# Optimization experiments

Hardware: AMD Instinct MI355X
Metric: run time of the kernel (lower is better)

The kernel has to match this reference:

```python
import jax, jax.numpy as jnp
import numpy as np

# --- static configuration (mirrors init_kwargs) ---
L = 16        # latent_size
HL = 512      # hypernet_layer_size
D = 64        # decoder_layer_size
NDEC = 2      # decoder_n_layers
B, G = 128, 100  # batch, grid (pressure levels)
LOGP_MEAN, LOGP_STD = 0.0, 3.0
T_MEAN, T_STD = 1500.0, 500.0

# decoder layer structure generated by the hypernet
WEIGHT_SIZES = [(1, D)] + [(D, D)] * NDEC + [(D, 1)]
BIAS_SIZES = [1] + [D] * NDEC + [1]
OUT_SIZE = sum(a * b for a, b in WEIGHT_SIZES) + sum(BIAS_SIZES)  # 8450


def setup_inputs() -> dict:
    key = jax.random.key(0)
    ks = jax.random.split(key, 8)
    def init(k, shape, fan_in):
        return (jax.random.normal(k, shape, jnp.float32) / np.float32(np.sqrt(fan_in)))
    return {
        "z": jax.random.normal(ks[0], (B, L), jnp.float32),
        "log_P": jax.random.normal(ks[1], (B, G), jnp.float32) * 2.0,
        # hypernet MLP params: L -> HL -> HL -> HL -> OUT_SIZE
        "hW0": init(ks[2], (L, HL), L), "hb0": jnp.zeros((HL,), jnp.float32),
        "hW1": init(ks[3], (HL, HL), HL), "hb1": jnp.zeros((HL,), jnp.float32),
        "hW2": init(ks[4], (HL, HL), HL), "hb2": jnp.zeros((HL,), jnp.float32),
        "hWo": init(ks[5], (HL, OUT_SIZE), HL), "hbo": jnp.zeros((OUT_SIZE,), jnp.float32),
    }


def reference(z, log_P, hW0, hb0, hW1, hb1, hW2, hb2, hWo, hbo):
    Bsz, Gsz = log_P.shape
    R = Bsz * Gsz  # flattened rows
    # broadcast latent over the pressure grid: (B, L) -> (R, L)
    z_flat = jnp.broadcast_to(z[:, None, :], (Bsz, Gsz, z.shape[-1])).reshape(R, -1)
    # normalize pressure -> decoder input, shape (R, 1)
    x = (log_P.reshape(R, 1) - LOGP_MEAN) / LOGP_STD
    # hypernet MLP (leaky_relu, slope 0.01 like torch default)
    h = jax.nn.leaky_relu(z_flat @ hW0 + hb0)
    h = jax.nn.leaky_relu(h @ hW1 + hb1)
    h = jax.nn.leaky_relu(h @ hW2 + hb2)
    wab = h @ hWo + hbo  # (R, OUT_SIZE): per-row decoder weights+biases
    # per-row decoder: chain of batched GEMVs with siren activation
    off = 0
    n_layers = len(WEIGHT_SIZES)
    for i, ((di, do), bs) in enumerate(zip(WEIGHT_SIZES, BIAS_SIZES)):
        n = di * do
        w = wab[:, off:off + n].reshape(R, di, do)
        b = wab[:, off + n:off + n + bs]  # broadcasts against (R, do)
        off += n + bs
        x = jnp.einsum('bi,bij->bj', x, w) + b
        if i == 0:
            x = x * 30.0  # siren first-layer omega_0
        if i < n_layers - 1:
            x = jnp.sin(x)  # siren activation; last layer is Identity
    T_pred = x.reshape(Bsz, Gsz)
    # undo temperature normalization
    return T_pred * T_STD + T_MEAN
```

## Files before the change

kernel.cpp:

```cpp
#include <hip/hip_runtime.h>

#define WSTRIDE 8704
#define GSTR 65

__device__ __forceinline__ float lrelu(float x) { return x > 0.0f ? x : 0.01f * x; }

__global__ __launch_bounds__(128) void h0T_kernel(const float* __restrict__ z,
                                                  const float* __restrict__ W,
                                                  const float* __restrict__ bias,
                                                  float* __restrict__ h0T) {
    int j = blockIdx.x;
    int b = threadIdx.x;
    float zr[16];
    *(float4*)&zr[0]  = *(const float4*)&z[b * 16 + 0];
    *(float4*)&zr[4]  = *(const float4*)&z[b * 16 + 4];
    *(float4*)&zr[8]  = *(const float4*)&z[b * 16 + 8];
    *(float4*)&zr[12] = *(const float4*)&z[b * 16 + 12];
    float acc = bias[j];
#pragma unroll
    for (int l = 0; l < 16; ++l) acc = fmaf(zr[l], W[l * 512 + j], acc);
    h0T[j * 128 + b] = lrelu(acc);
}

__global__ __launch_bounds__(256) void gemmT_kernel(const float* __restrict__ At,
                                                    const float* __restrict__ W,
                                                    const float* __restrict__ bias,
                                                    float* __restrict__ OT) {
    __shared__ __align__(16) float As[512][4];
    __shared__ float red[4][64][5];
    int jt = blockIdx.x & 7;
    int bt = blockIdx.x >> 3;
    int tid = threadIdx.x;
    int lane = tid & 63;
    int wid  = __builtin_amdgcn_readfirstlane(tid >> 6);
    int b0 = bt * 4;
#pragma unroll
    for (int r = 0; r < 4; ++r) {
        int p = r * 256 + tid;
        int k = p >> 1, q = p & 1;
        *(float2*)&As[k][q * 2] = *(const float2*)&At[k * 128 + b0 + q * 2];
    }
    __syncthreads();
    int j = jt * 64 + lane;
    float acc[4] = {};
    int k0 = wid * 128;
#pragma unroll 8
    for (int kk = 0; kk < 128; ++kk) {
        int k = k0 + kk;
        float4 a = *(const float4*)&As[k][0];
        float w = W[k * 512 + j];
        acc[0] = fmaf(a.x, w, acc[0]);
        acc[1] = fmaf(a.y, w, acc[1]);
        acc[2] = fmaf(a.z, w, acc[2]);
        acc[3] = fmaf(a.w, w, acc[3]);
    }
#pragma unroll
    for (int i = 0; i < 4; ++i) red[wid][lane][i] = acc[i];
    __syncthreads();
    int jj = tid >> 2;
    int bb = tid & 3;
    float s = red[0][jj][bb] + red[1][jj][bb] + red[2][jj][bb] + red[3][jj][bb];
    int jg = jt * 64 + jj;
    OT[jg * 128 + b0 + bb] = lrelu(s + bias[jg]);
}

__global__ __launch_bounds__(256) void wabT_kernel(const float* __restrict__ At,
                                                   const float* __restrict__ W,
                                                   const float* __restrict__ bias,
                                                   float* __restrict__ wab) {
    __shared__ __align__(16) float As[512][16];
    __shared__ float red[4][64][33];
    int tid = threadIdx.x;
    if (blockIdx.x == 528) {
        int b = tid & 127;
        int jc = 8448 + (tid >> 7);
        float a0 = 0.f, a1 = 0.f, a2 = 0.f, a3 = 0.f;
#pragma unroll 4
        for (int k4 = 0; k4 < 128; ++k4) {
            a0 = fmaf(At[(k4*4+0) * 128 + b], W[(k4*4+0) * 8450 + jc], a0);
            a1 = fmaf(At[(k4*4+1) * 128 + b], W[(k4*4+1) * 8450 + jc], a1);
            a2 = fmaf(At[(k4*4+2) * 128 + b], W[(k4*4+2) * 8450 + jc], a2);
            a3 = fmaf(At[(k4*4+3) * 128 + b], W[(k4*4+3) * 8450 + jc], a3);
        }
        wab[b * WSTRIDE + jc] = a0 + a1 + a2 + a3 + bias[jc];
        return;
    }
    int v = (blockIdx.x & 7) * 66 + (blockIdx.x >> 3);
    int jt = v >> 3;
    int bt = v & 7;
    int lane = tid & 63;
    int wid  = __builtin_amdgcn_readfirstlane(tid >> 6);
    int b0 = bt * 16;
#pragma unroll
    for (int r = 0; r < 16; ++r) {
        int p = r * 256 + tid;
        int k = p >> 3, q = p & 7;
        *(float2*)&As[k][q * 2] = *(const float2*)&At[k * 128 + b0 + q * 2];
    }
    __syncthreads();
    int j0 = jt * 128 + lane * 2;
    float acc[16][2] = {};
    int k0 = wid * 128;
#pragma unroll 4
    for (int kk = 0; kk < 128; ++kk) {
        int k = k0 + kk;
        float4 a0 = *(const float4*)&As[k][0];
        float4 a1 = *(const float4*)&As[k][4];
        float4 a2 = *(const float4*)&As[k][8];
        float4 a3 = *(const float4*)&As[k][12];
        float2 w = *(const float2*)&W[k * 8450 + j0];
        float av[16] = {a0.x,a0.y,a0.z,a0.w, a1.x,a1.y,a1.z,a1.w,
                        a2.x,a2.y,a2.z,a2.w, a3.x,a3.y,a3.z,a3.w};
#pragma unroll
        for (int bb = 0; bb < 16; ++bb) {
            acc[bb][0] = fmaf(av[bb], w.x, acc[bb][0]);
            acc[bb][1] = fmaf(av[bb], w.y, acc[bb][1]);
        }
    }
#pragma unroll
    for (int bb = 0; bb < 16; ++bb) {
        red[wid][lane][bb * 2 + 0] = acc[bb][0];
        red[wid][lane][bb * 2 + 1] = acc[bb][1];
    }
    __syncthreads();
    int jj = tid >> 1;
    int bh = tid & 1;
    int lane_r = jj >> 1;
    int jl = jj & 1;
    int jg = jt * 128 + jj;
    float bj = bias[jg];
#pragma unroll
    for (int bq = 0; bq < 8; ++bq) {
        int bb = bh * 8 + bq;
        int idx = bb * 2 + jl;
        float s = red[0][lane_r][idx] + red[1][lane_r][idx]
                + red[2][lane_r][idx] + red[3][lane_r][idx];
        wab[(b0 + bb) * WSTRIDE + jg] = s + bj;
    }
}

__global__ __launch_bounds__(256) void decoder_kernel(const float* __restrict__ wab,
                                                      const float* __restrict__ logP,
                                                      float* __restrict__ out) {
    __shared__ __align__(16) float Wl[64 * 64];
    __shared__ float hX[64 * GSTR];
    __shared__ float hY[64 * GSTR];
    __shared__ float red[4][68];
    int b   = blockIdx.x >> 1;
    int gbl = blockIdx.x & 1;
    int tid = threadIdx.x;
    int lane = tid & 63;
    int wid  = __builtin_amdgcn_readfirstlane(tid >> 6);
    int jq = wid * 16;
    int g = gbl * 64 + lane;
    bool act = g < 100;
    const float* __restrict__ row = wab + b * WSTRIDE;
    float x0 = act ? logP[b * 100 + g] * (1.0f / 3.0f) : 0.0f;

    float c0 = row[64];
#pragma unroll
    for (int t = 0; t < 16; ++t)
        hX[(jq + t) * GSTR + lane] = __sinf(30.0f * fmaf(x0, row[jq + t], c0));
#pragma unroll
    for (int r = 0; r < 16; ++r) {
        int idx = r * 256 + tid;
        Wl[idx] = row[65 + idx];
    }
    __syncthreads();

    {
        float a[16];
#pragma unroll
        for (int t = 0; t < 16; ++t) a[t] = row[4161 + jq + t];
#pragma unroll 4
        for (int i = 0; i < 64; ++i) {
            float hi = hX[i * GSTR + lane];
            const float* wr = &Wl[i * 64 + jq];
            float4 w0 = *(const float4*)&wr[0];
            float4 w1 = *(const float4*)&wr[4];
            float4 w2 = *(const float4*)&wr[8];
            float4 w3 = *(const float4*)&wr[12];
            a[0]  = fmaf(hi, w0.x, a[0]);  a[1]  = fmaf(hi, w0.y, a[1]);
            a[2]  = fmaf(hi, w0.z, a[2]);  a[3]  = fmaf(hi, w0.w, a[3]);
            a[4]  = fmaf(hi, w1.x, a[4]);  a[5]  = fmaf(hi, w1.y, a[5]);
            a[6]  = fmaf(hi, w1.z, a[6]);  a[7]  = fmaf(hi, w1.w, a[7]);
            a[8]  = fmaf(hi, w2.x, a[8]);  a[9]  = fmaf(hi, w2.y, a[9]);
            a[10] = fmaf(hi, w2.z, a[10]); a[11] = fmaf(hi, w2.w, a[11]);
            a[12] = fmaf(hi, w3.x, a[12]); a[13] = fmaf(hi, w3.y, a[13]);
            a[14] = fmaf(hi, w3.z, a[14]); a[15] = fmaf(hi, w3.w, a[15]);
        }
#pragma unroll
        for (int t = 0; t < 16; ++t) hY[(jq + t) * GSTR + lane] = __sinf(a[t]);
    }
    __syncthreads();
#pragma unroll
    for (int r = 0; r < 16; ++r) {
        int idx = r * 256 + tid;
        Wl[idx] = row[4225 + idx];
    }
    __syncthreads();

    {
        float a[16];
#pragma unroll
        for (int t = 0; t < 16; ++t) a[t] = row[8321 + jq + t];
#pragma unroll 4
        for (int i = 0; i < 64; ++i) {
            float hi = hY[i * GSTR + lane];
            const float* wr = &Wl[i * 64 + jq];
            float4 w0 = *(const float4*)&wr[0];
            float4 w1 = *(const float4*)&wr[4];
            float4 w2 = *(const float4*)&wr[8];
            float4 w3 = *(const float4*)&wr[12];
            a[0]  = fmaf(hi, w0.x, a[0]);  a[1]  = fmaf(hi, w0.y, a[1]);
            a[2]  = fmaf(hi, w0.z, a[2]);  a[3]  = fmaf(hi, w0.w, a[3]);
            a[4]  = fmaf(hi, w1.x, a[4]);  a[5]  = fmaf(hi, w1.y, a[5]);
            a[6]  = fmaf(hi, w1.z, a[6]);  a[7]  = fmaf(hi, w1.w, a[7]);
            a[8]  = fmaf(hi, w2.x, a[8]);  a[9]  = fmaf(hi, w2.y, a[9]);
            a[10] = fmaf(hi, w2.z, a[10]); a[11] = fmaf(hi, w2.w, a[11]);
            a[12] = fmaf(hi, w3.x, a[12]); a[13] = fmaf(hi, w3.y, a[13]);
            a[14] = fmaf(hi, w3.z, a[14]); a[15] = fmaf(hi, w3.w, a[15]);
        }
#pragma unroll
        for (int t = 0; t < 16; ++t) hX[(jq + t) * GSTR + lane] = __sinf(a[t]);
    }
    __syncthreads();

    float p = 0.f;
#pragma unroll
    for (int t = 0; t < 16; ++t)
        p = fmaf(hX[(jq + t) * GSTR + lane], row[8385 + jq + t], p);
    red[wid][lane] = p;
    __syncthreads();
    if (wid == 0 && act) {
        float s = red[0][lane] + red[1][lane] + red[2][lane] + red[3][lane] + row[8449];
        out[b * 100 + g] = fmaf(s, 500.0f, 1500.0f);
    }
}

extern "C" void kernel_launch(void* const* d_in, const int* in_sizes, int n_in,
                              void* d_out, int out_size, void* d_ws, size_t ws_size,
                              hipStream_t stream) {
    const float* z    = (const float*)d_in[0];
    const float* logP = (const float*)d_in[1];
    const float* hW0  = (const float*)d_in[2];
    const float* hb0  = (const float*)d_in[3];
    const float* hW1  = (const float*)d_in[4];
    const float* hb1  = (const float*)d_in[5];
    const float* hW2  = (const float*)d_in[6];
    const float* hb2  = (const float*)d_in[7];
    const float* hWo  = (const float*)d_in[8];
    const float* hbo  = (const float*)d_in[9];
    float* out = (float*)d_out;

    float* wab = (float*)d_ws;
    float* h0T = wab + 128 * WSTRIDE;
    float* h1T = h0T + 512 * 128;
    float* h2T = h1T + 512 * 128;

    h0T_kernel<<<512, 128, 0, stream>>>(z, hW0, hb0, h0T);
    gemmT_kernel<<<256, 256, 0, stream>>>(h0T, hW1, hb1, h1T);
    gemmT_kernel<<<256, 256, 0, stream>>>(h1T, hW2, hb2, h2T);
    wabT_kernel<<<529, 256, 0, stream>>>(h2T, hWo, hbo, wab);
    decoder_kernel<<<256, 256, 0, stream>>>(wab, logP, out);
}
```

Baseline: 72.71 us.

## Double threads in gemm/decoder, software-pipeline wab GEMM, fold tail columns into tiles

The hidden-layer GEMMs and the decoder now use 512-thread blocks, so each wave handles half the K range or half the output columns, with a wider final reduction. The wab GEMM inner loop is restructured into a double-buffered register pipeline that prefetches the next 4-k group of shared-memory A values and global W values while computing the current one. It also gets a 2-blocks-per-SIMD launch bound. The special block for the two leftover columns is replaced by an extra tile-column with clamped loads and guarded stores. Together these aim to raise parallelism and hide load latency, at the cost of more registers in the wab kernel and more reduction work.

New measurement: 61.08 us. 16.0% less time.

```diff
diff --git a/kernel.cpp b/kernel.cpp
--- a/kernel.cpp
+++ b/kernel.cpp
@@ -22,12 +22,12 @@
     h0T[j * 128 + b] = lrelu(acc);
 }
 
-__global__ __launch_bounds__(256) void gemmT_kernel(const float* __restrict__ At,
+__global__ __launch_bounds__(512) void gemmT_kernel(const float* __restrict__ At,
                                                     const float* __restrict__ W,
                                                     const float* __restrict__ bias,
                                                     float* __restrict__ OT) {
     __shared__ __align__(16) float As[512][4];
-    __shared__ float red[4][64][5];
+    __shared__ float red[8][64][5];
     int jt = blockIdx.x & 7;
     int bt = blockIdx.x >> 3;
     int tid = threadIdx.x;
@@ -35,17 +35,17 @@
     int wid  = __builtin_amdgcn_readfirstlane(tid >> 6);
     int b0 = bt * 4;
 #pragma unroll
-    for (int r = 0; r < 4; ++r) {
-        int p = r * 256 + tid;
+    for (int r = 0; r < 2; ++r) {
+        int p = r * 512 + tid;
         int k = p >> 1, q = p & 1;
         *(float2*)&As[k][q * 2] = *(const float2*)&At[k * 128 + b0 + q * 2];
     }
     __syncthreads();
     int j = jt * 64 + lane;
     float acc[4] = {};
-    int k0 = wid * 128;
+    int k0 = wid * 64;
 #pragma unroll 8
-    for (int kk = 0; kk < 128; ++kk) {
+    for (int kk = 0; kk < 64; ++kk) {
         int k = k0 + kk;
         float4 a = *(const float4*)&As[k][0];
         float w = W[k * 512 + j];
@@ -57,35 +57,57 @@
 #pragma unroll
     for (int i = 0; i < 4; ++i) red[wid][lane][i] = acc[i];
     __syncthreads();
-    int jj = tid >> 2;
-    int bb = tid & 3;
-    float s = red[0][jj][bb] + red[1][jj][bb] + red[2][jj][bb] + red[3][jj][bb];
-    int jg = jt * 64 + jj;
-    OT[jg * 128 + b0 + bb] = lrelu(s + bias[jg]);
-}
-
-__global__ __launch_bounds__(256) void wabT_kernel(const float* __restrict__ At,
-                                                   const float* __restrict__ W,
-                                                   const float* __restrict__ bias,
-                                                   float* __restrict__ wab) {
+    if (tid < 256) {
+        int jj = tid >> 2;
+        int bb = tid & 3;
+        float s = 0.f;
+#pragma unroll
+        for (int w = 0; w < 8; ++w) s += red[w][jj][bb];
+        int jg = jt * 64 + jj;
+        OT[jg * 128 + b0 + bb] = lrelu(s + bias[jg]);
+    }
+}
+
+__device__ __forceinline__ void loadg(const float As[][16], const float* __restrict__ W,
+                                      int k0, int g, int j0,
+                                      float4 (&aa)[4][4], float2 (&ww)[4]) {
+    int kb = k0 + g * 4;
+#pragma unroll
+    for (int kk = 0; kk < 4; ++kk) {
+        const float* asr = As[kb + kk];
+        aa[kk][0] = *(const float4*)&asr[0];
+        aa[kk][1] = *(const float4*)&asr[4];
+        aa[kk][2] = *(const float4*)&asr[8];
+        aa[kk][3] = *(const float4*)&asr[12];
+        ww[kk] = *(const float2*)&W[(kb + kk) * 8450 + j0];
+    }
+}
+
+__device__ __forceinline__ void compg(const float4 (&aa)[4][4], const float2 (&ww)[4],
+                                      float (&acc)[16][2]) {
+#pragma unroll
+    for (int kk = 0; kk < 4; ++kk) {
+#pragma unroll
+        for (int q = 0; q < 4; ++q) {
+            const float4 a = aa[kk][q];
+            const float av[4] = {a.x, a.y, a.z, a.w};
+#pragma unroll
+            for (int e = 0; e < 4; ++e) {
+                acc[q * 4 + e][0] = fmaf(av[e], ww[kk].x, acc[q * 4 + e][0]);
+                acc[q * 4 + e][1] = fmaf(av[e], ww[kk].y, acc[q * 4 + e][1]);
+            }
+        }
+    }
+}
+
+__global__ __launch_bounds__(256, 2) void wabT_kernel(const float* __restrict__ At,
+                                                      const float* __restrict__ W,
+                                                      const float* __restrict__ bias,
+                                                      float* __restrict__ wab) {
     __shared__ __align__(16) float As[512][16];
     __shared__ float red[4][64][33];
     int tid = threadIdx.x;
-    if (blockIdx.x == 528) {
-        int b = tid & 127;
-        int jc = 8448 + (tid >> 7);
-        float a0 = 0.f, a1 = 0.f, a2 = 0.f, a3 = 0.f;
-#pragma unroll 4
-        for (int k4 = 0; k4 < 128; ++k4) {
-            a0 = fmaf(At[(k4*4+0) * 128 + b], W[(k4*4+0) * 8450 + jc], a0);
-            a1 = fmaf(At[(k4*4+1) * 128 + b], W[(k4*4+1) * 8450 + jc], a1);
-            a2 = fmaf(At[(k4*4+2) * 128 + b], W[(k4*4+2) * 8450 + jc], a2);
-            a3 = fmaf(At[(k4*4+3) * 128 + b], W[(k4*4+3) * 8450 + jc], a3);
-        }
-        wab[b * WSTRIDE + jc] = a0 + a1 + a2 + a3 + bias[jc];
-        return;
-    }
-    int v = (blockIdx.x & 7) * 66 + (blockIdx.x >> 3);
+    int v = (blockIdx.x & 7) * 67 + (blockIdx.x >> 3);
     int jt = v >> 3;
     int bt = v & 7;
     int lane = tid & 63;
@@ -98,25 +120,22 @@
         *(float2*)&As[k][q * 2] = *(const float2*)&At[k * 128 + b0 + q * 2];
     }
     __syncthreads();
-    int j0 = jt * 128 + lane * 2;
+    int j0r = jt * 128 + lane * 2;
+    int j0 = j0r < 8448 ? j0r : 8448;
     float acc[16][2] = {};
     int k0 = wid * 128;
-#pragma unroll 4
-    for (int kk = 0; kk < 128; ++kk) {
-        int k = k0 + kk;
-        float4 a0 = *(const float4*)&As[k][0];
-        float4 a1 = *(const float4*)&As[k][4];
-        float4 a2 = *(const float4*)&As[k][8];
-        float4 a3 = *(const float4*)&As[k][12];
-        float2 w = *(const float2*)&W[k * 8450 + j0];
-        float av[16] = {a0.x,a0.y,a0.z,a0.w, a1.x,a1.y,a1.z,a1.w,
-                        a2.x,a2.y,a2.z,a2.w, a3.x,a3.y,a3.z,a3.w};
-#pragma unroll
-        for (int bb = 0; bb < 16; ++bb) {
-            acc[bb][0] = fmaf(av[bb], w.x, acc[bb][0]);
-            acc[bb][1] = fmaf(av[bb], w.y, acc[bb][1]);
-        }
-    }
+    float4 aA[4][4], aB[4][4];
+    float2 wA[4], wB[4];
+    loadg(As, W, k0, 0, j0, aA, wA);
+    for (int it = 0; it < 15; ++it) {
+        loadg(As, W, k0, 2 * it + 1, j0, aB, wB);
+        compg(aA, wA, acc);
+        loadg(As, W, k0, 2 * it + 2, j0, aA, wA);
+        compg(aB, wB, acc);
+    }
+    loadg(As, W, k0, 31, j0, aB, wB);
+    compg(aA, wA, acc);
+    compg(aB, wB, acc);
 #pragma unroll
     for (int bb = 0; bb < 16; ++bb) {
         red[wid][lane][bb * 2 + 0] = acc[bb][0];
@@ -128,30 +147,32 @@
     int lane_r = jj >> 1;
     int jl = jj & 1;
     int jg = jt * 128 + jj;
-    float bj = bias[jg];
-#pragma unroll
-    for (int bq = 0; bq < 8; ++bq) {
-        int bb = bh * 8 + bq;
-        int idx = bb * 2 + jl;
-        float s = red[0][lane_r][idx] + red[1][lane_r][idx]
-                + red[2][lane_r][idx] + red[3][lane_r][idx];
-        wab[(b0 + bb) * WSTRIDE + jg] = s + bj;
-    }
-}
-
-__global__ __launch_bounds__(256) void decoder_kernel(const float* __restrict__ wab,
+    if (jg < 8450) {
+        float bj = bias[jg];
+#pragma unroll
+        for (int bq = 0; bq < 8; ++bq) {
+            int bb = bh * 8 + bq;
+            int idx = bb * 2 + jl;
+            float s = red[0][lane_r][idx] + red[1][lane_r][idx]
+                    + red[2][lane_r][idx] + red[3][lane_r][idx];
+            wab[(b0 + bb) * WSTRIDE + jg] = s + bj;
+        }
+    }
+}
+
+__global__ __launch_bounds__(512) void decoder_kernel(const float* __restrict__ wab,
                                                       const float* __restrict__ logP,
                                                       float* __restrict__ out) {
     __shared__ __align__(16) float Wl[64 * 64];
     __shared__ float hX[64 * GSTR];
     __shared__ float hY[64 * GSTR];
-    __shared__ float red[4][68];
+    __shared__ float red[8][68];
     int b   = blockIdx.x >> 1;
     int gbl = blockIdx.x & 1;
     int tid = threadIdx.x;
     int lane = tid & 63;
     int wid  = __builtin_amdgcn_readfirstlane(tid >> 6);
-    int jq = wid * 16;
+    int jq = wid * 8;
     int g = gbl * 64 + lane;
     bool act = g < 100;
     const float* __restrict__ row = wab + b * WSTRIDE;
@@ -159,81 +180,71 @@
 
     float c0 = row[64];
 #pragma unroll
-    for (int t = 0; t < 16; ++t)
+    for (int t = 0; t < 8; ++t)
         hX[(jq + t) * GSTR + lane] = __sinf(30.0f * fmaf(x0, row[jq + t], c0));
 #pragma unroll
-    for (int r = 0; r < 16; ++r) {
-        int idx = r * 256 + tid;
+    for (int r = 0; r < 8; ++r) {
+        int idx = r * 512 + tid;
         Wl[idx] = row[65 + idx];
     }
     __syncthreads();
 
     {
-        float a[16];
-#pragma unroll
-        for (int t = 0; t < 16; ++t) a[t] = row[4161 + jq + t];
-#pragma unroll 4
+        float a[8];
+#pragma unroll
+        for (int t = 0; t < 8; ++t) a[t] = row[4161 + jq + t];
+#pragma unroll 8
         for (int i = 0; i < 64; ++i) {
             float hi = hX[i * GSTR + lane];
             const float* wr = &Wl[i * 64 + jq];
             float4 w0 = *(const float4*)&wr[0];
             float4 w1 = *(const float4*)&wr[4];
-            float4 w2 = *(const float4*)&wr[8];
-            float4 w3 = *(const float4*)&wr[12];
-            a[0]  = fmaf(hi, w0.x, a[0]);  a[1]  = fmaf(hi, w0.y, a[1]);
-            a[2]  = fmaf(hi, w0.z, a[2]);  a[3]  = fmaf(hi, w0.w, a[3]);
-            a[4]  = fmaf(hi, w1.x, a[4]);  a[5]  = fmaf(hi, w1.y, a[5]);
-            a[6]  = fmaf(hi, w1.z, a[6]);  a[7]  = fmaf(hi, w1.w, a[7]);
-            a[8]  = fmaf(hi, w2.x, a[8]);  a[9]  = fmaf(hi, w2.y, a[9]);
-            a[10] = fmaf(hi, w2.z, a[10]); a[11] = fmaf(hi, w2.w, a[11]);
-            a[12] = fmaf(hi, w3.x, a[12]); a[13] = fmaf(hi, w3.y, a[13]);
-            a[14] = fmaf(hi, w3.z, a[14]); a[15] = fmaf(hi, w3.w, a[15]);
-        }
-#pragma unroll
-        for (int t = 0; t < 16; ++t) hY[(jq + t) * GSTR + lane] = __sinf(a[t]);
-    }
-    __syncthreads();
-#pragma unroll
-    for (int r = 0; r < 16; ++r) {
-        int idx = r * 256 + tid;
+            a[0] = fmaf(hi, w0.x, a[0]);  a[1] = fmaf(hi, w0.y, a[1]);
+            a[2] = fmaf(hi, w0.z, a[2]);  a[3] = fmaf(hi, w0.w, a[3]);
+            a[4] = fmaf(hi, w1.x, a[4]);  a[5] = fmaf(hi, w1.y, a[5]);
+            a[6] = fmaf(hi, w1.z, a[6]);  a[7] = fmaf(hi, w1.w, a[7]);
+        }
+#pragma unroll
+        for (int t = 0; t < 8; ++t) hY[(jq + t) * GSTR + lane] = __sinf(a[t]);
+    }
+    __syncthreads();
+#pragma unroll
+    for (int r = 0; r < 8; ++r) {
+        int idx = r * 512 + tid;
         Wl[idx] = row[4225 + idx];
     }
     __syncthreads();
 
     {
-        float a[16];
-#pragma unroll
-        for (int t = 0; t < 16; ++t) a[t] = row[8321 + jq + t];
-#pragma unroll 4
+        float a[8];
+#pragma unroll
+        for (int t = 0; t < 8; ++t) a[t] = row[8321 + jq + t];
+#pragma unroll 8
         for (int i = 0; i < 64; ++i) {
             float hi = hY[i * GSTR + lane];
             const float* wr = &Wl[i * 64 + jq];
             float4 w0 = *(const float4*)&wr[0];
             float4 w1 = *(const float4*)&wr[4];
-            float4 w2 = *(const float4*)&wr[8];
-            float4 w3 = *(const float4*)&wr[12];
-            a[0]  = fmaf(hi, w0.x, a[0]);  a[1]  = fmaf(hi, w0.y, a[1]);
-            a[2]  = fmaf(hi, w0.z, a[2]);  a[3]  = fmaf(hi, w0.w, a[3]);
-            a[4]  = fmaf(hi, w1.x, a[4]);  a[5]  = fmaf(hi, w1.y, a[5]);
-            a[6]  = fmaf(hi, w1.z, a[6]);  a[7]  = fmaf(hi, w1.w, a[7]);
-            a[8]  = fmaf(hi, w2.x, a[8]);  a[9]  = fmaf(hi, w2.y, a[9]);
-            a[10] = fmaf(hi, w2.z, a[10]); a[11] = fmaf(hi, w2.w, a[11]);
-            a[12] = fmaf(hi, w3.x, a[12]); a[13] = fmaf(hi, w3.y, a[13]);
-            a[14] = fmaf(hi, w3.z, a[14]); a[15] = fmaf(hi, w3.w, a[15]);
-        }
-#pragma unroll
-        for (int t = 0; t < 16; ++t) hX[(jq + t) * GSTR + lane] = __sinf(a[t]);
+            a[0] = fmaf(hi, w0.x, a[0]);  a[1] = fmaf(hi, w0.y, a[1]);
+            a[2] = fmaf(hi, w0.z, a[2]);  a[3] = fmaf(hi, w0.w, a[3]);
+            a[4] = fmaf(hi, w1.x, a[4]);  a[5] = fmaf(hi, w1.y, a[5]);
+            a[6] = fmaf(hi, w1.z, a[6]);  a[7] = fmaf(hi, w1.w, a[7]);
+        }
+#pragma unroll
+        for (int t = 0; t < 8; ++t) hX[(jq + t) * GSTR + lane] = __sinf(a[t]);
     }
     __syncthreads();
 
     float p = 0.f;
 #pragma unroll
-    for (int t = 0; t < 16; ++t)
+    for (int t = 0; t < 8; ++t)
         p = fmaf(hX[(jq + t) * GSTR + lane], row[8385 + jq + t], p);
     red[wid][lane] = p;
     __syncthreads();
     if (wid == 0 && act) {
-        float s = red[0][lane] + red[1][lane] + red[2][lane] + red[3][lane] + row[8449];
+        float s = row[8449];
+#pragma unroll
+        for (int w = 0; w < 8; ++w) s += red[w][lane];
         out[b * 100 + g] = fmaf(s, 500.0f, 1500.0f);
     }
 }
@@ -259,8 +270,8 @@
     float* h2T = h1T + 512 * 128;
 
     h0T_kernel<<<512, 128, 0, stream>>>(z, hW0, hb0, h0T);
-    gemmT_kernel<<<256, 256, 0, stream>>>(h0T, hW1, hb1, h1T);
-    gemmT_kernel<<<256, 256, 0, stream>>>(h1T, hW2, hb2, h2T);
-    wabT_kernel<<<529, 256, 0, stream>>>(h2T, hWo, hbo, wab);
-    decoder_kernel<<<256, 256, 0, stream>>>(wab, logP, out);
-}
+    gemmT_kernel<<<256, 512, 0, stream>>>(h0T, hW1, hb1, h1T);
+    gemmT_kernel<<<256, 512, 0, stream>>>(h1T, hW2, hb2, h2T);
+    wabT_kernel<<<536, 256, 0, stream>>>(h2T, hWo, hbo, wab);
+    decoder_kernel<<<256, 512, 0, stream>>>(wab, logP, out);
+}
```

## Drop LDS staging in GEMMs, software-pipeline wab loads, read decoder weights from global

Applied to the files above, without the earlier changes.

The hidden GEMMs now read activations directly from global memory instead of staging them in LDS, and use 512 threads with an 8-way K split. The output GEMM drops its separate tail block by clamping columns, adds a manual 4-deep register prefetch pipeline, and writes wab with a 3-float pad after the first bias so the decoder's 64x64 weight rows are 16-byte aligned. The decoder then reads those weights straight from global/L2 with float4 loads instead of copying them into LDS, which removes several barriers. The risk is more global traffic and higher register pressure in exchange for less LDS and fewer synchronisations.

Result: slower. 107.3 us (+47.6%).

```diff
diff --git a/kernel.cpp b/kernel.cpp
--- a/kernel.cpp
+++ b/kernel.cpp
@@ -1,7 +1,6 @@
 #include <hip/hip_runtime.h>
 
 #define WSTRIDE 8704
-#define GSTR 65
 
 __device__ __forceinline__ float lrelu(float x) { return x > 0.0f ? x : 0.01f * x; }
 
@@ -22,33 +21,28 @@
     h0T[j * 128 + b] = lrelu(acc);
 }
 
-__global__ __launch_bounds__(256) void gemmT_kernel(const float* __restrict__ At,
-                                                    const float* __restrict__ W,
-                                                    const float* __restrict__ bias,
-                                                    float* __restrict__ OT) {
-    __shared__ __align__(16) float As[512][4];
-    __shared__ float red[4][64][5];
+__global__ __launch_bounds__(512, 2) void gemmT_kernel(const float* __restrict__ At,
+                                                       const float* __restrict__ W,
+                                                       const float* __restrict__ bias,
+                                                       float* __restrict__ OT) {
+    __shared__ float red[8][64][5];
     int jt = blockIdx.x & 7;
     int bt = blockIdx.x >> 3;
     int tid = threadIdx.x;
     int lane = tid & 63;
-    int wid  = __builtin_amdgcn_readfirstlane(tid >> 6);
+    int widv = tid >> 6;
+    asm volatile("v_mov_b32 %0, %0" : "+v"(widv));
+    int wid = __builtin_amdgcn_readfirstlane(tid >> 6);
     int b0 = bt * 4;
-#pragma unroll
-    for (int r = 0; r < 4; ++r) {
-        int p = r * 256 + tid;
-        int k = p >> 1, q = p & 1;
-        *(float2*)&As[k][q * 2] = *(const float2*)&At[k * 128 + b0 + q * 2];
-    }
-    __syncthreads();
     int j = jt * 64 + lane;
+    int k0 = widv * 64;
+    const float* __restrict__ Ap = At + (size_t)k0 * 128 + b0;
+    const float* __restrict__ Wp = W + (size_t)k0 * 512 + j;
     float acc[4] = {};
-    int k0 = wid * 128;
 #pragma unroll 8
-    for (int kk = 0; kk < 128; ++kk) {
-        int k = k0 + kk;
-        float4 a = *(const float4*)&As[k][0];
-        float w = W[k * 512 + j];
+    for (int kk = 0; kk < 64; ++kk) {
+        float4 a = *(const float4*)(Ap + (size_t)kk * 128);
+        float w = Wp[(size_t)kk * 512];
         acc[0] = fmaf(a.x, w, acc[0]);
         acc[1] = fmaf(a.y, w, acc[1]);
         acc[2] = fmaf(a.z, w, acc[2]);
@@ -57,125 +51,118 @@
 #pragma unroll
     for (int i = 0; i < 4; ++i) red[wid][lane][i] = acc[i];
     __syncthreads();
-    int jj = tid >> 2;
-    int bb = tid & 3;
-    float s = red[0][jj][bb] + red[1][jj][bb] + red[2][jj][bb] + red[3][jj][bb];
-    int jg = jt * 64 + jj;
-    OT[jg * 128 + b0 + bb] = lrelu(s + bias[jg]);
-}
-
-__global__ __launch_bounds__(256) void wabT_kernel(const float* __restrict__ At,
-                                                   const float* __restrict__ W,
-                                                   const float* __restrict__ bias,
-                                                   float* __restrict__ wab) {
-    __shared__ __align__(16) float As[512][16];
+    if (tid < 256) {
+        int jj = tid >> 2;
+        int bb = tid & 3;
+        float s = 0.f;
+#pragma unroll
+        for (int w = 0; w < 8; ++w) s += red[w][jj][bb];
+        int jg = jt * 64 + jj;
+        OT[jg * 128 + b0 + bb] = lrelu(s + bias[jg]);
+    }
+}
+
+__global__ __launch_bounds__(256, 2) void wabT_kernel(const float* __restrict__ At,
+                                                      const float* __restrict__ W,
+                                                      const float* __restrict__ bias,
+                                                      float* __restrict__ wab) {
     __shared__ float red[4][64][33];
     int tid = threadIdx.x;
-    if (blockIdx.x == 528) {
-        int b = tid & 127;
-        int jc = 8448 + (tid >> 7);
-        float a0 = 0.f, a1 = 0.f, a2 = 0.f, a3 = 0.f;
-#pragma unroll 4
-        for (int k4 = 0; k4 < 128; ++k4) {
-            a0 = fmaf(At[(k4*4+0) * 128 + b], W[(k4*4+0) * 8450 + jc], a0);
-            a1 = fmaf(At[(k4*4+1) * 128 + b], W[(k4*4+1) * 8450 + jc], a1);
-            a2 = fmaf(At[(k4*4+2) * 128 + b], W[(k4*4+2) * 8450 + jc], a2);
-            a3 = fmaf(At[(k4*4+3) * 128 + b], W[(k4*4+3) * 8450 + jc], a3);
-        }
-        wab[b * WSTRIDE + jc] = a0 + a1 + a2 + a3 + bias[jc];
-        return;
-    }
-    int v = (blockIdx.x & 7) * 66 + (blockIdx.x >> 3);
+    int lane = tid & 63;
+    int widv = tid >> 6;
+    asm volatile("v_mov_b32 %0, %0" : "+v"(widv));
+    int wid = __builtin_amdgcn_readfirstlane(tid >> 6);
+    int v = (blockIdx.x & 7) * 67 + (blockIdx.x >> 3);
     int jt = v >> 3;
     int bt = v & 7;
-    int lane = tid & 63;
-    int wid  = __builtin_amdgcn_readfirstlane(tid >> 6);
     int b0 = bt * 16;
-#pragma unroll
-    for (int r = 0; r < 16; ++r) {
-        int p = r * 256 + tid;
-        int k = p >> 3, q = p & 7;
-        *(float2*)&As[k][q * 2] = *(const float2*)&At[k * 128 + b0 + q * 2];
-    }
-    __syncthreads();
-    int j0 = jt * 128 + lane * 2;
-    float acc[16][2] = {};
-    int k0 = wid * 128;
-#pragma unroll 4
-    for (int kk = 0; kk < 128; ++kk) {
-        int k = k0 + kk;
-        float4 a0 = *(const float4*)&As[k][0];
-        float4 a1 = *(const float4*)&As[k][4];
-        float4 a2 = *(const float4*)&As[k][8];
-        float4 a3 = *(const float4*)&As[k][12];
-        float2 w = *(const float2*)&W[k * 8450 + j0];
-        float av[16] = {a0.x,a0.y,a0.z,a0.w, a1.x,a1.y,a1.z,a1.w,
-                        a2.x,a2.y,a2.z,a2.w, a3.x,a3.y,a3.z,a3.w};
-#pragma unroll
-        for (int bb = 0; bb < 16; ++bb) {
-            acc[bb][0] = fmaf(av[bb], w.x, acc[bb][0]);
-            acc[bb][1] = fmaf(av[bb], w.y, acc[bb][1]);
-        }
-    }
-#pragma unroll
-    for (int bb = 0; bb < 16; ++bb) {
-        red[wid][lane][bb * 2 + 0] = acc[bb][0];
-        red[wid][lane][bb * 2 + 1] = acc[bb][1];
-    }
-    __syncthreads();
-    int jj = tid >> 1;
-    int bh = tid & 1;
-    int lane_r = jj >> 1;
-    int jl = jj & 1;
-    int jg = jt * 128 + jj;
-    float bj = bias[jg];
-#pragma unroll
-    for (int bq = 0; bq < 8; ++bq) {
-        int bb = bh * 8 + bq;
-        int idx = bb * 2 + jl;
-        float s = red[0][lane_r][idx] + red[1][lane_r][idx]
-                + red[2][lane_r][idx] + red[3][lane_r][idx];
-        wab[(b0 + bb) * WSTRIDE + jg] = s + bj;
+    int j0r = jt * 128 + lane * 2;
+    int j0 = j0r < 8448 ? j0r : 8448;
+    int k0 = widv * 128;
+    const float* __restrict__ Ap = At + (size_t)k0 * 128 + b0;
+    const float* __restrict__ Wp = W + (size_t)k0 * 8450 + j0;
+    float acc[16][2];
+#pragma unroll
+    for (int i = 0; i < 16; ++i) { acc[i][0] = 0.f; acc[i][1] = 0.f; }
+
+#define LDK(A, Wv, kk) do {                                     \
+        const float* ap_ = Ap + (size_t)(kk) * 128;             \
+        *(float4*)&A[0]  = *(const float4*)(ap_ + 0);           \
+        *(float4*)&A[4]  = *(const float4*)(ap_ + 4);           \
+        *(float4*)&A[8]  = *(const float4*)(ap_ + 8);           \
+        *(float4*)&A[12] = *(const float4*)(ap_ + 12);          \
+        Wv = *(const float2*)(Wp + (size_t)(kk) * 8450);        \
+    } while (0)
+#define FMAK(A, Wv) do {                                        \
+        _Pragma("unroll")                                       \
+        for (int i_ = 0; i_ < 16; ++i_) {                       \
+            acc[i_][0] = fmaf(A[i_], Wv.x, acc[i_][0]);         \
+            acc[i_][1] = fmaf(A[i_], Wv.y, acc[i_][1]);         \
+        }                                                       \
+    } while (0)
+
+    float s0[16], s1[16], s2[16], s3[16];
+    float2 u0, u1, u2, u3;
+    LDK(s0, u0, 0); LDK(s1, u1, 1); LDK(s2, u2, 2); LDK(s3, u3, 3);
+    for (int base = 0; base < 124; base += 4) {
+        FMAK(s0, u0); LDK(s0, u0, base + 4);
+        FMAK(s1, u1); LDK(s1, u1, base + 5);
+        FMAK(s2, u2); LDK(s2, u2, base + 6);
+        FMAK(s3, u3); LDK(s3, u3, base + 7);
+    }
+    FMAK(s0, u0); FMAK(s1, u1); FMAK(s2, u2); FMAK(s3, u3);
+#undef LDK
+#undef FMAK
+
+#pragma unroll
+    for (int i = 0; i < 16; ++i) {
+        red[wid][lane][i * 2 + 0] = acc[i][0];
+        red[wid][lane][i * 2 + 1] = acc[i][1];
+    }
+    __syncthreads();
+    int q = tid >> 6;
+    int ls = tid & 63;
+    int jb = jt * 128 + ls * 2;
+#pragma unroll
+    for (int m = 0; m < 8; ++m) {
+        int idx = q * 8 + m;
+        float s = red[0][ls][idx] + red[1][ls][idx]
+                + red[2][ls][idx] + red[3][ls][idx];
+        int bb = b0 + (idx >> 1);
+        int jlog = jb + (idx & 1);
+        if (jlog < 8450)
+            wab[(size_t)bb * WSTRIDE + jlog + (jlog >= 65 ? 3 : 0)] = s + bias[jlog];
     }
 }
 
 __global__ __launch_bounds__(256) void decoder_kernel(const float* __restrict__ wab,
                                                       const float* __restrict__ logP,
                                                       float* __restrict__ out) {
-    __shared__ __align__(16) float Wl[64 * 64];
-    __shared__ float hX[64 * GSTR];
-    __shared__ float hY[64 * GSTR];
+    __shared__ float hX[64 * 65];
+    __shared__ float hY[64 * 65];
     __shared__ float red[4][68];
-    int b   = blockIdx.x >> 1;
-    int gbl = blockIdx.x & 1;
+    int b  = blockIdx.x >> 1;
+    int gh = blockIdx.x & 1;
     int tid = threadIdx.x;
     int lane = tid & 63;
-    int wid  = __builtin_amdgcn_readfirstlane(tid >> 6);
-    int jq = wid * 16;
-    int g = gbl * 64 + lane;
+    int jq = (tid >> 6) * 16;
+    int g = gh * 64 + lane;
     bool act = g < 100;
-    const float* __restrict__ row = wab + b * WSTRIDE;
+    const float* __restrict__ row = wab + (size_t)b * WSTRIDE;
     float x0 = act ? logP[b * 100 + g] * (1.0f / 3.0f) : 0.0f;
-
     float c0 = row[64];
 #pragma unroll
     for (int t = 0; t < 16; ++t)
-        hX[(jq + t) * GSTR + lane] = __sinf(30.0f * fmaf(x0, row[jq + t], c0));
-#pragma unroll
-    for (int r = 0; r < 16; ++r) {
-        int idx = r * 256 + tid;
-        Wl[idx] = row[65 + idx];
-    }
-    __syncthreads();
-
+        hX[(jq + t) * 65 + lane] = __sinf(30.0f * fmaf(x0, row[jq + t], c0));
+    __syncthreads();
     {
         float a[16];
 #pragma unroll
-        for (int t = 0; t < 16; ++t) a[t] = row[4161 + jq + t];
+        for (int t = 0; t < 16; ++t) a[t] = row[4164 + jq + t];
 #pragma unroll 4
         for (int i = 0; i < 64; ++i) {
-            float hi = hX[i * GSTR + lane];
-            const float* wr = &Wl[i * 64 + jq];
+            float hi = hX[i * 65 + lane];
+            const float* wr = row + 68 + i * 64 + jq;
             float4 w0 = *(const float4*)&wr[0];
             float4 w1 = *(const float4*)&wr[4];
             float4 w2 = *(const float4*)&wr[8];
@@ -190,24 +177,17 @@
             a[14] = fmaf(hi, w3.z, a[14]); a[15] = fmaf(hi, w3.w, a[15]);
         }
 #pragma unroll
-        for (int t = 0; t < 16; ++t) hY[(jq + t) * GSTR + lane] = __sinf(a[t]);
-    }
-    __syncthreads();
-#pragma unroll
-    for (int r = 0; r < 16; ++r) {
-        int idx = r * 256 + tid;
-        Wl[idx] = row[4225 + idx];
-    }
-    __syncthreads();
-
+        for (int t = 0; t < 16; ++t) hY[(jq + t) * 65 + lane] = __sinf(a[t]);
+    }
+    __syncthreads();
     {
         float a[16];
 #pragma unroll
-        for (int t = 0; t < 16; ++t) a[t] = row[8321 + jq + t];
+        for (int t = 0; t < 16; ++t) a[t] = row[8324 + jq + t];
 #pragma unroll 4
         for (int i = 0; i < 64; ++i) {
-            float hi = hY[i * GSTR + lane];
-            const float* wr = &Wl[i * 64 + jq];
+            float hi = hY[i * 65 + lane];
+            const float* wr = row + 4228 + i * 64 + jq;
             float4 w0 = *(const float4*)&wr[0];
             float4 w1 = *(const float4*)&wr[4];
             float4 w2 = *(const float4*)&wr[8];
@@ -222,18 +202,17 @@
             a[14] = fmaf(hi, w3.z, a[14]); a[15] = fmaf(hi, w3.w, a[15]);
         }
 #pragma unroll
-        for (int t = 0; t < 16; ++t) hX[(jq + t) * GSTR + lane] = __sinf(a[t]);
-    }
-    __syncthreads();
-
+        for (int t = 0; t < 16; ++t) hX[(jq + t) * 65 + lane] = __sinf(a[t]);
+    }
+    __syncthreads();
     float p = 0.f;
 #pragma unroll
     for (int t = 0; t < 16; ++t)
-        p = fmaf(hX[(jq + t) * GSTR + lane], row[8385 + jq + t], p);
-    red[wid][lane] = p;
-    __syncthreads();
-    if (wid == 0 && act) {
-        float s = red[0][lane] + red[1][lane] + red[2][lane] + red[3][lane] + row[8449];
+        p = fmaf(hX[(jq + t) * 65 + lane], row[8388 + jq + t], p);
+    red[tid >> 6][lane] = p;
+    __syncthreads();
+    if (tid < 64 && act) {
+        float s = red[0][lane] + red[1][lane] + red[2][lane] + red[3][lane] + row[8452];
         out[b * 100 + g] = fmaf(s, 500.0f, 1500.0f);
     }
 }
@@ -259,8 +238,8 @@
     float* h2T = h1T + 512 * 128;
 
     h0T_kernel<<<512, 128, 0, stream>>>(z, hW0, hb0, h0T);
-    gemmT_kernel<<<256, 256, 0, stream>>>(h0T, hW1, hb1, h1T);
-    gemmT_kernel<<<256, 256, 0, stream>>>(h1T, hW2, hb2, h2T);
-    wabT_kernel<<<529, 256, 0, stream>>>(h2T, hWo, hbo, wab);
+    gemmT_kernel<<<256, 512, 0, stream>>>(h0T, hW1, hb1, h1T);
+    gemmT_kernel<<<256, 512, 0, stream>>>(h1T, hW2, hb2, h2T);
+    wabT_kernel<<<536, 256, 0, stream>>>(h2T, hWo, hbo, wab);
     decoder_kernel<<<256, 256, 0, stream>>>(wab, logP, out);
 }
```
